# Kernel tuning notes

Measured on AMD Instinct MI355X. Metric: run time of the kernel, lower is better.

## Reference

```python
import math
import jax, jax.numpy as jnp
import numpy as np

N_FEATURES = 32
DEGREE = 3
BATCH = 8192
N_POLY = math.comb(N_FEATURES + DEGREE, DEGREE)  # 6545


def _build_monomial_indices(n_features, degree):
    """Static (numpy) indices replicating the Pascal-triangle recursion in TaylorMap._poly.

    For degree level i (i = 1..degree-1), the original code appends, for each feature f,
    x[:, f] * prev_block[:, :comb(i+f, i)].  We flatten that into gather index arrays so the
    whole block is one vectorized gather+multiply instead of a Python loop of slices/concats.
    """
    levels = []
    for i in range(1, degree):
        counts = np.array([math.comb(i + f, i) for f in range(n_features)], dtype=np.int64)
        f_idx = np.repeat(np.arange(n_features, dtype=np.int64), counts)
        m_idx = np.concatenate([np.arange(c, dtype=np.int64) for c in counts])
        levels.append((f_idx, m_idx))
    return levels

_LEVELS = _build_monomial_indices(N_FEATURES, DEGREE)


def _poly(x):
    # x: [B, n].  Returns [B, n_poly] monomial features in the exact order of TaylorMap._poly.
    b = x.shape[0]
    parts = [jnp.ones((b, 1), x.dtype), x]
    prev = x
    for f_idx, m_idx in _LEVELS:  # static loop over degree levels (degree-1 iterations)
        new = x[:, f_idx] * prev[:, m_idx]  # [B, comb(n+i, i+1)-ish block]
        parts.append(new)
        prev = new
    return jnp.concatenate(parts, axis=-1)


def setup_inputs() -> dict:
    key = jax.random.key(0)
    kx, kw = jax.random.split(key)
    x = jax.random.normal(kx, (BATCH, N_FEATURES), dtype=jnp.float32)
    # learned weight W: [n_poly, n_features] (default init is zeros; use small randn for a
    # non-degenerate numerical baseline)
    W = jax.random.normal(kw, (N_POLY, N_FEATURES), dtype=jnp.float32) * 0.02
    return {"x": x, "W": W}


def reference(x, W):
    # TaylorMap(x) = x * residual + poly(x) @ W   (residual=True)
    return x + _poly(x) @ W
```

## Files before the change

### kernel.cpp

```cpp
#include <hip/hip_runtime.h>
#include <cstdint>
#include <cstddef>
#include <utility>


#define NF 32
#define NPOLY 6545
#define NSTEPS 417
#define NOCT 834
#define NDESC 1024
#define TSTRIDE 576
#define D2OFF 40
#define XDSTRIDE 34

#define T_BYTES   36864
#define XD_OFF    36864
#define SMEM_BYTES 39040

typedef _Float16 f16x8 __attribute__((ext_vector_type(8)));
typedef float f32x16 __attribute__((ext_vector_type(16)));

#define D2N 528
struct D2I { uint8_t a[D2N]; uint8_t b[D2N]; };
constexpr D2I build_d2i() {
    D2I t{};
    int k = 0;
    for (int f = 0; f < NF; ++f)
        for (int m = 0; m <= f; ++m) { t.a[k] = (uint8_t)f; t.b[k] = (uint8_t)m; ++k; }
    return t;
}
constexpr D2I D2T = build_d2i();

struct Desc { uint32_t d[NDESC]; };
constexpr Desc build_desc() {
    Desc D{};
    int u = 0;
    for (int o = 0; o < 72; ++o)
        D.d[u++] = (uint32_t)(o * 16);
    for (int f = 0; f < NF; ++f) {
        int cnt = (f + 1) * (f + 2) / 2;
        for (int j8 = 0; j8 < (cnt + 7) / 8; ++j8)
            D.d[u++] = (uint32_t)((D2OFF + 8 * j8) * 2) | ((uint32_t)((1 + f) * 2) << 16);
    }
    while (u < NDESC) D.d[u++] = 0u;
    return D;
}
__device__ const Desc DESC_G = build_desc();

struct Oldk { int16_t v[NSTEPS * 16]; };
constexpr Oldk build_oldk() {
    Oldk K{};
    int k = 0;
    for (int ti = 0; ti < 576; ++ti) {
        int old;
        if (ti == 0) old = 0;
        else if (ti <= 32) old = ti;
        else if (ti >= D2OFF && ti < D2OFF + D2N) old = 33 + (ti - D2OFF);
        else old = -1;
        K.v[k++] = (int16_t)old;
    }
    for (int f = 0; f < NF; ++f) {
        int cnt = (f + 1) * (f + 2) / 2;
        int off3 = 0;
        for (int g = 0; g < f; ++g) off3 += (g + 1) * (g + 2) / 2;
        int oc = (cnt + 7) / 8;
        for (int m = 0; m < oc * 8; ++m)
            K.v[k++] = (int16_t)(m < cnt ? 561 + off3 + m : -1);
    }
    return K;
}
__device__ const Oldk OLDK_G = build_oldk();

template<int TI>
__device__ __forceinline__ _Float16 tval(const float (&xr)[NF]) {
    if constexpr (TI == 0) return (_Float16)1.0f;
    else if constexpr (TI >= 1 && TI <= 32) return (_Float16)xr[TI - 1];
    else if constexpr (TI >= D2OFF && TI < D2OFF + D2N) {
        constexpr int m = TI - D2OFF;
        return (_Float16)(xr[D2T.a[m]] * xr[D2T.b[m]]);
    } else return (_Float16)0.0f;
}

template<int O, int... Js>
__device__ __forceinline__ void put_oct(std::integer_sequence<int, Js...>,
                                        const float (&xr)[NF], _Float16* trow, int r) {
    f16x8 v = { tval<O * 8 + Js>(xr)... };
    int slot = (O & ~7) | ((O ^ r) & 7);
    *(f16x8*)(trow + slot * 8) = v;
}

template<int BASE, int... Os>
__device__ __forceinline__ void p1_octs(std::integer_sequence<int, Os...>,
                                        const float (&xr)[NF], _Float16* trow, int r) {
    (put_oct<BASE + Os>(std::make_integer_sequence<int, 8>{}, xr, trow, r), ...);
}

template<int V>
__device__ __forceinline__ void xdw(const float (&xr)[NF], _Float16* xdrow) {
    if constexpr (V == 0) xdrow[0] = (_Float16)1.0f;
    else if constexpr (V <= 32) xdrow[V] = (_Float16)xr[V - 1];
}

template<int G>
__device__ __forceinline__ void p1_group(const float (&xr)[NF], _Float16* trow,
                                         _Float16* xdrow, int r) {
    if constexpr (G < 8)
        p1_octs<G * 5>(std::make_integer_sequence<int, 5>{}, xr, trow, r);
    else
        p1_octs<40 + (G - 8) * 4>(std::make_integer_sequence<int, 4>{}, xr, trow, r);
    xdw<2 * G>(xr, xdrow);
    xdw<2 * G + 1>(xr, xdrow);
    if constexpr (G == 15) xdw<32>(xr, xdrow);
}

__global__ void prep(const float* __restrict__ x, const float* __restrict__ W,
                     float* __restrict__ out, _Float16* __restrict__ Wh) {
    int b = blockIdx.x;
    if (b < 256) {
        int id = b * 256 + threadIdx.x;
        ((float4*)out)[id] = ((const float4*)x)[id];
    } else {
        int id = (b - 256) * 256 + threadIdx.x;
        if (id < NSTEPS * 64) {
            int step = id >> 6, rem = id & 63, hs = rem >> 5, n = rem & 31;
            int k0 = step * 16 + hs * 8;
            f16x8 v;
#pragma unroll
            for (int j = 0; j < 8; ++j) {
                int old = OLDK_G.v[k0 + j];
                v[j] = (_Float16)(old >= 0 ? W[old * 32 + n] : 0.0f);
            }
            *(f16x8*)(Wh + (size_t)id * 8) = v;
        }
    }
}

__global__ __launch_bounds__(512, 2) void gemm(const float* __restrict__ x,
                                               const _Float16* __restrict__ Wh,
                                               float* __restrict__ out) {
    __shared__ __align__(16) unsigned char smem[SMEM_BYTES];
    _Float16* t  = (_Float16*)smem;
    _Float16* xd = (_Float16*)(smem + XD_OFF);

    const int tid = threadIdx.x;
    const int wave = __builtin_amdgcn_readfirstlane(tid >> 6);
    const int lane = tid & 63;
    const int hsel = lane >> 5, r = lane & 31;
    const int mtile = blockIdx.x >> 1;
    const int kh = blockIdx.x & 1;

    {
        const int pr = tid & 31, g = tid >> 5;
        float xr[NF];
        const float4* xp = (const float4*)(x + (size_t)(mtile * 32 + pr) * NF);
#pragma unroll
        for (int i = 0; i < 8; ++i) {
            float4 v = xp[i];
            xr[4 * i + 0] = v.x; xr[4 * i + 1] = v.y;
            xr[4 * i + 2] = v.z; xr[4 * i + 3] = v.w;
        }
        _Float16* trow = t + pr * TSTRIDE;
        _Float16* xdrow = xd + pr * XDSTRIDE;
        switch (g) {
            case  0: p1_group< 0>(xr, trow, xdrow, pr); break;
            case  1: p1_group< 1>(xr, trow, xdrow, pr); break;
            case  2: p1_group< 2>(xr, trow, xdrow, pr); break;
            case  3: p1_group< 3>(xr, trow, xdrow, pr); break;
            case  4: p1_group< 4>(xr, trow, xdrow, pr); break;
            case  5: p1_group< 5>(xr, trow, xdrow, pr); break;
            case  6: p1_group< 6>(xr, trow, xdrow, pr); break;
            case  7: p1_group< 7>(xr, trow, xdrow, pr); break;
            case  8: p1_group< 8>(xr, trow, xdrow, pr); break;
            case  9: p1_group< 9>(xr, trow, xdrow, pr); break;
            case 10: p1_group<10>(xr, trow, xdrow, pr); break;
            case 11: p1_group<11>(xr, trow, xdrow, pr); break;
            case 12: p1_group<12>(xr, trow, xdrow, pr); break;
            case 13: p1_group<13>(xr, trow, xdrow, pr); break;
            case 14: p1_group<14>(xr, trow, xdrow, pr); break;
            default: p1_group<15>(xr, trow, xdrow, pr); break;
        }
    }

    const int c = kh * 8 + wave;
    const int s0 = __builtin_amdgcn_readfirstlane((c * NSTEPS) >> 4);
    const int s1 = __builtin_amdgcn_readfirstlane(((c + 1) * NSTEPS) >> 4);
    int didx = 2 * (s0 + lane);
    uint32_t vD0 = DESC_G.d[didx];
    uint32_t vD1 = DESC_G.d[didx + 1];

    __syncthreads();

    const char* trowB = (const char*)t + r * (TSTRIDE * 2);
    const char* xdrowB = (const char*)xd + r * (XDSTRIDE * 2);
    const char* wpB = (const char*)Wh + lane * 16;
    const uint32_t rx = (uint32_t)((r & 7) << 4);

    f32x16 acc0, acc1;
#pragma unroll
    for (int i = 0; i < 16; ++i) { acc0[i] = 0.0f; acc1[i] = 0.0f; }

#define DSEL(IDX) (hsel ? __builtin_amdgcn_readlane(vD1, (IDX)) \
                        : __builtin_amdgcn_readlane(vD0, (IDX)))

    uint32_t dp0 = DSEL(0);
    uint32_t dp1 = DSEL(1);
    f16x8 araw0 = *(const f16x8*)(trowB + ((dp0 & 0xffffu) ^ rx));
    _Float16 xs0 = *(const _Float16*)(xdrowB + (dp0 >> 16));
    f16x8 araw1 = *(const f16x8*)(trowB + ((dp1 & 0xffffu) ^ rx));
    _Float16 xs1 = *(const _Float16*)(xdrowB + (dp1 >> 16));
    f16x8 breg0 = *(const f16x8*)(wpB + (size_t)s0 * 1024);
    f16x8 breg1 = *(const f16x8*)(wpB + (size_t)(s0 + 1) * 1024);

#define BODY(P, SCUR) do {                                                    \
    f16x8 xsv_ = { xs##P, xs##P, xs##P, xs##P, xs##P, xs##P, xs##P, xs##P };  \
    f16x8 a_ = araw##P * xsv_;                                                \
    f16x8 bu_ = breg##P;                                                      \
    uint32_t dn_ = DSEL((SCUR) + 2 - s0);                                     \
    araw##P = *(const f16x8*)(trowB + ((dn_ & 0xffffu) ^ rx));                \
    xs##P   = *(const _Float16*)(xdrowB + (dn_ >> 16));                       \
    breg##P = *(const f16x8*)(wpB + (size_t)((SCUR) + 2) * 1024);             \
    acc##P = __builtin_amdgcn_mfma_f32_32x32x16_f16(a_, bu_, acc##P, 0, 0, 0);\
} while (0)

    int s = s0;
    for (; s + 1 < s1; s += 2) { BODY(0, s); BODY(1, s + 1); }
    if (s < s1) {
        f16x8 xsv_ = { xs0, xs0, xs0, xs0, xs0, xs0, xs0, xs0 };
        f16x8 a_ = araw0 * xsv_;
        acc0 = __builtin_amdgcn_mfma_f32_32x32x16_f16(a_, breg0, acc0, 0, 0, 0);
    }
#undef BODY
#undef DSEL

    __syncthreads();
    float* red = (float*)smem;
    float* bank = red + wave * 1024;
#pragma unroll
    for (int reg = 0; reg < 16; ++reg) {
        int rr = (reg & 3) + 8 * (reg >> 2) + 4 * hsel;
        bank[rr * 32 + r] = acc0[reg] + acc1[reg];
    }
    __syncthreads();
    float* op = out + (size_t)mtile * 1024;
#pragma unroll
    for (int i = 0; i < 2; ++i) {
        int e = tid + i * 512;
        float v = red[e] + red[1024 + e] + red[2048 + e] + red[3072 + e]
                + red[4096 + e] + red[5120 + e] + red[6144 + e] + red[7168 + e];
        atomicAdd(op + e, v);
    }
}

extern "C" void kernel_launch(void* const* d_in, const int* in_sizes, int n_in,
                              void* d_out, int out_size, void* d_ws, size_t ws_size,
                              hipStream_t stream) {
    (void)in_sizes; (void)n_in; (void)out_size; (void)ws_size;
    const float* x = (const float*)d_in[0];
    const float* W = (const float*)d_in[1];
    float* out = (float*)d_out;
    _Float16* Wh = (_Float16*)d_ws;

    prep<<<361, 256, 0, stream>>>(x, W, out, Wh);
    gemm<<<512, 512, 0, stream>>>(x, Wh, out);
}
```

Baseline: 69.97 us.

## Pad K steps to uniform chunks and deepen MFMA prefetch pipeline

Pads the K dimension from 417 to 448 steps with zero weights so each of the 16 wave-chunks gets exactly 28 steps. This replaces variable-length loops with a fully unrolled loop that prefetches operands four steps ahead. It merges the two accumulators into one and raises the launch-bounds occupancy hint to 4 blocks. The aim is better latency hiding and no loop overhead. In exchange it adds about 7% padded MFMA work, makes every MFMA depend on the previous one through the single accumulator, and may squeeze registers under the tighter launch bound.

```diff
diff --git a/kernel.cpp b/kernel.cpp
--- a/kernel.cpp
+++ b/kernel.cpp
@@ -6,14 +6,15 @@
 
 #define NF 32
 #define NPOLY 6545
-#define NSTEPS 417
+#define NSTEPS 448
+#define NREAL 417
 #define NOCT 834
 #define NDESC 1024
+#define CHUNK 28
 #define TSTRIDE 576
 #define D2OFF 40
 #define XDSTRIDE 34
 
-#define T_BYTES   36864
 #define XD_OFF    36864
 #define SMEM_BYTES 39040
 
@@ -67,6 +68,7 @@
         for (int m = 0; m < oc * 8; ++m)
             K.v[k++] = (int16_t)(m < cnt ? 561 + off3 + m : -1);
     }
+    while (k < NSTEPS * 16) K.v[k++] = (int16_t)-1;
     return K;
 }
 __device__ const Oldk OLDK_G = build_oldk();
@@ -135,7 +137,7 @@
     }
 }
 
-__global__ __launch_bounds__(512, 2) void gemm(const float* __restrict__ x,
+__global__ __launch_bounds__(512, 4) void gemm(const float* __restrict__ x,
                                                const _Float16* __restrict__ Wh,
                                                float* __restrict__ out) {
     __shared__ __align__(16) unsigned char smem[SMEM_BYTES];
@@ -182,11 +184,9 @@
     }
 
     const int c = kh * 8 + wave;
-    const int s0 = __builtin_amdgcn_readfirstlane((c * NSTEPS) >> 4);
-    const int s1 = __builtin_amdgcn_readfirstlane(((c + 1) * NSTEPS) >> 4);
-    int didx = 2 * (s0 + lane);
-    uint32_t vD0 = DESC_G.d[didx];
-    uint32_t vD1 = DESC_G.d[didx + 1];
+    const int s0 = __builtin_amdgcn_readfirstlane(c * CHUNK);
+    uint32_t vD0 = DESC_G.d[2 * (s0 + lane)];
+    uint32_t vD1 = DESC_G.d[2 * (s0 + lane) + 1];
 
     __syncthreads();
 
@@ -195,41 +195,43 @@
     const char* wpB = (const char*)Wh + lane * 16;
     const uint32_t rx = (uint32_t)((r & 7) << 4);
 
-    f32x16 acc0, acc1;
-#pragma unroll
-    for (int i = 0; i < 16; ++i) { acc0[i] = 0.0f; acc1[i] = 0.0f; }
+    f32x16 acc;
+#pragma unroll
+    for (int i = 0; i < 16; ++i) acc[i] = 0.0f;
 
 #define DSEL(IDX) (hsel ? __builtin_amdgcn_readlane(vD1, (IDX)) \
                         : __builtin_amdgcn_readlane(vD0, (IDX)))
 
-    uint32_t dp0 = DSEL(0);
-    uint32_t dp1 = DSEL(1);
-    f16x8 araw0 = *(const f16x8*)(trowB + ((dp0 & 0xffffu) ^ rx));
-    _Float16 xs0 = *(const _Float16*)(xdrowB + (dp0 >> 16));
-    f16x8 araw1 = *(const f16x8*)(trowB + ((dp1 & 0xffffu) ^ rx));
-    _Float16 xs1 = *(const _Float16*)(xdrowB + (dp1 >> 16));
-    f16x8 breg0 = *(const f16x8*)(wpB + (size_t)s0 * 1024);
-    f16x8 breg1 = *(const f16x8*)(wpB + (size_t)(s0 + 1) * 1024);
-
-#define BODY(P, SCUR) do {                                                    \
+    f16x8 araw0, araw1, araw2, araw3;
+    f16x8 breg0, breg1, breg2, breg3;
+    _Float16 xs0, xs1, xs2, xs3;
+
+#define LOADSLOT(P, IDX) do {                                                 \
+    uint32_t d_ = DSEL(IDX);                                                  \
+    araw##P = *(const f16x8*)(trowB + ((d_ & 0xffffu) ^ rx));                 \
+    xs##P   = *(const _Float16*)(xdrowB + (d_ >> 16));                        \
+    breg##P = *(const f16x8*)(wpB + (size_t)(s0 + (IDX)) * 1024);             \
+} while (0)
+
+    LOADSLOT(0, 0); LOADSLOT(1, 1); LOADSLOT(2, 2); LOADSLOT(3, 3);
+
+#define BODY(P, IDX) do {                                                     \
     f16x8 xsv_ = { xs##P, xs##P, xs##P, xs##P, xs##P, xs##P, xs##P, xs##P };  \
     f16x8 a_ = araw##P * xsv_;                                                \
     f16x8 bu_ = breg##P;                                                      \
-    uint32_t dn_ = DSEL((SCUR) + 2 - s0);                                     \
-    araw##P = *(const f16x8*)(trowB + ((dn_ & 0xffffu) ^ rx));                \
-    xs##P   = *(const _Float16*)(xdrowB + (dn_ >> 16));                       \
-    breg##P = *(const f16x8*)(wpB + (size_t)((SCUR) + 2) * 1024);             \
-    acc##P = __builtin_amdgcn_mfma_f32_32x32x16_f16(a_, bu_, acc##P, 0, 0, 0);\
+    LOADSLOT(P, (IDX) + 4);   \
+    acc = __builtin_amdgcn_mfma_f32_32x32x16_f16(a_, bu_, acc, 0, 0, 0);      \
 } while (0)
 
-    int s = s0;
-    for (; s + 1 < s1; s += 2) { BODY(0, s); BODY(1, s + 1); }
-    if (s < s1) {
-        f16x8 xsv_ = { xs0, xs0, xs0, xs0, xs0, xs0, xs0, xs0 };
-        f16x8 a_ = araw0 * xsv_;
-        acc0 = __builtin_amdgcn_mfma_f32_32x32x16_f16(a_, breg0, acc0, 0, 0, 0);
+#pragma unroll
+    for (int i = 0; i < 7; ++i) {
+        BODY(0, 4 * i + 0);
+        BODY(1, 4 * i + 1);
+        BODY(2, 4 * i + 2);
+        BODY(3, 4 * i + 3);
     }
 #undef BODY
+#undef LOADSLOT
 #undef DSEL
 
     __syncthreads();
@@ -238,7 +240,7 @@
 #pragma unroll
     for (int reg = 0; reg < 16; ++reg) {
         int rr = (reg & 3) + 8 * (reg >> 2) + 4 * hsel;
-        bank[rr * 32 + r] = acc0[reg] + acc1[reg];
+        bank[rr * 32 + r] = acc[reg];
     }
     __syncthreads();
     float* op = out + (size_t)mtile * 1024;
@@ -260,6 +262,6 @@
     float* out = (float*)d_out;
     _Float16* Wh = (_Float16*)d_ws;
 
-    prep<<<361, 256, 0, stream>>>(x, W, out, Wh);
+    prep<<<368, 256, 0, stream>>>(x, W, out, Wh);
     gemm<<<512, 512, 0, stream>>>(x, Wh, out);
 }
```

New measurement: 69.58 us. About the same (-0.6%).
